# Kernel optimization log

Measured on AMD Instinct MI355X. Metric: run time of the kernel, lower is better.

## Reference

```python
import jax, jax.numpy as jnp
import numpy as np
import math

D_MODEL = 768
D_STATE = 16
EXPAND = 2
D_CONV = 4
D_INNER = EXPAND * D_MODEL  # 1536
DT_RANK = math.ceil(D_MODEL / 16)  # 48
BATCH = 2
SEQ = 2048


def setup_inputs() -> dict:
    key = jax.random.key(0)
    ks = jax.random.split(key, 9)
    s = lambda fan_in: 1.0 / np.sqrt(fan_in)
    x = jax.random.normal(ks[0], (BATCH, SEQ, D_MODEL), dtype=jnp.float32)
    W_in = jax.random.normal(ks[1], (D_MODEL, 2 * D_INNER), dtype=jnp.float32) * s(D_MODEL)
    conv_w = jax.random.normal(ks[2], (D_INNER, 1, D_CONV), dtype=jnp.float32) * s(D_CONV)
    conv_b = jax.random.normal(ks[3], (D_INNER,), dtype=jnp.float32) * s(D_CONV)
    W_x = jax.random.normal(ks[4], (D_INNER, DT_RANK + 2 * D_STATE), dtype=jnp.float32) * s(D_INNER)
    W_dt = jax.random.normal(ks[5], (DT_RANK, D_INNER), dtype=jnp.float32) * s(DT_RANK)
    b_dt = jax.random.normal(ks[6], (D_INNER,), dtype=jnp.float32) * s(DT_RANK)
    A_log = jnp.log(jnp.tile(jnp.arange(1, D_STATE + 1, dtype=jnp.float32), (D_INNER, 1)))
    Dp = jnp.ones((D_INNER,), dtype=jnp.float32)
    W_out = jax.random.normal(ks[7], (D_INNER, D_MODEL), dtype=jnp.float32) * s(D_INNER)
    return {"x": x, "W_in": W_in, "conv_w": conv_w, "conv_b": conv_b,
            "W_x": W_x, "W_dt": W_dt, "b_dt": b_dt, "A_log": A_log,
            "Dp": Dp, "W_out": W_out}


def _mamba_forward(x, W_in, conv_w, conv_b, W_x, W_dt, b_dt, A_log, Dp, W_out):
    B, L, _ = x.shape
    xz = x @ W_in                                   # [B,L,2E]
    u, res = jnp.split(xz, [D_INNER], axis=-1)      # [B,L,E] each

    # Depthwise causal conv1d (padding=d_conv-1 on the left, truncated to L)
    u_ncl = jnp.transpose(u, (0, 2, 1))             # [B,E,L]
    u_ncl = jax.lax.conv_general_dilated(
        u_ncl, conv_w,
        window_strides=(1,), padding=[(D_CONV - 1, 0)],
        dimension_numbers=("NCH", "OIH", "NCH"),
        feature_group_count=D_INNER)
    u_ncl = u_ncl + conv_b[None, :, None]
    u = jnp.transpose(u_ncl, (0, 2, 1))             # [B,L,E]
    u = jax.nn.silu(u)

    ssm = u @ W_x                                   # [B,L,R+2N]
    dt_raw, Bm, Cm = jnp.split(ssm, [DT_RANK, DT_RANK + D_STATE], axis=-1)
    dt = jax.nn.softplus(dt_raw @ W_dt + b_dt)      # [B,L,E]

    A = -jnp.exp(A_log)                             # [E,N]
    dA = jnp.exp(dt[..., None] * A)                 # [B,L,E,N]
    dBu = dt[..., None] * Bm[:, :, None, :] * u[..., None]  # [B,L,E,N]

    # Sequential SSM recurrence: h_t = dA_t * h_{t-1} + dBu_t; y_t = <h_t, C_t>
    def step(h, inp):
        dA_t, dBu_t, C_t = inp                      # [B,E,N],[B,E,N],[B,N]
        h = dA_t * h + dBu_t
        y_t = jnp.sum(h * C_t[:, None, :], axis=-1)  # [B,E]
        return h, y_t

    h0 = jnp.zeros((B, D_INNER, D_STATE), dtype=u.dtype)
    xs = (jnp.transpose(dA, (1, 0, 2, 3)),
          jnp.transpose(dBu, (1, 0, 2, 3)),
          jnp.transpose(Cm, (1, 0, 2)))
    _, ys = jax.lax.scan(step, h0, xs)              # [L,B,E]
    y = jnp.transpose(ys, (1, 0, 2))                # [B,L,E]

    y = y + u * Dp
    y = y * jax.nn.silu(res)
    return y @ W_out                                # [B,L,d_model]


def reference(x, W_in, conv_w, conv_b, W_x, W_dt, b_dt, A_log, Dp, W_out):
    return _mamba_forward(x, W_in, conv_w, conv_b, W_x, W_dt, b_dt, A_log, Dp, W_out)
```

## Files before the change

kernel.cpp:

```cpp
#include <hip/hip_runtime.h>
#include <hip/hip_bf16.h>
#include <math.h>

#define D_MODEL 768
#define D_STATE 16
#define D_CONV  4
#define D_INNER 1536
#define DT_RANK 48
#define BATCH   2
#define SEQ     2048
#define BL      (BATCH*SEQ)
#define XZ_W    (2*D_INNER)
#define SSM_W   (DT_RANK + 2*D_STATE)
#define BC_W    (2*D_STATE)
#define KSPLIT  12

#define NREC    (BATCH*D_INNER*D_STATE)
#define EG      (D_INNER/128)
#define CH      64
#define CT      32

typedef __attribute__((ext_vector_type(8))) short short8;
typedef __attribute__((ext_vector_type(4))) float f32x4;

__device__ __forceinline__ float silu_f(float x) { return x / (1.f + __expf(-x)); }
__device__ __forceinline__ float softplus_f(float x) {
    return fmaxf(x, 0.f) + log1pf(__expf(-fabsf(x)));
}

__device__ __forceinline__ void qpow8(float q, int half, float* qp)
{
    qp[0] = q;
    qp[1] = q * q;
    qp[2] = qp[1] * q;
    qp[3] = qp[1] * qp[1];
    qp[4] = qp[3] * q;
    qp[5] = qp[3] * qp[1];
    qp[6] = qp[3] * qp[2];
    qp[7] = qp[3] * qp[3];
    float s = half ? qp[7] : 1.0f;
    #pragma unroll
    for (int n = 0; n < 8; ++n) qp[n] *= s;
}

#define GLOAD16(g, l)                                                          \
    __builtin_amdgcn_global_load_lds(                                          \
        (const __attribute__((address_space(1))) unsigned int*)(g),            \
        (__attribute__((address_space(3))) unsigned int*)(l), 16, 0, 0)

#define GEMM128_BODY(A, Bt, K)                                                 \
    __shared__ __hip_bfloat16 As[128 * 32];                                    \
    __shared__ __hip_bfloat16 Bs[128 * 32];                                    \
    const int t    = threadIdx.x;                                              \
    const int wave = t >> 6;                                                   \
    const int lane = t & 63;                                                   \
    const int m0 = blockIdx.y * 128, n0 = blockIdx.x * 128;                    \
    const int wm = (wave >> 1) * 64, wn = (wave & 1) * 64;                     \
    const int l  = lane & 15, kq = lane >> 4;                                  \
    const int arow = t >> 2;                                                   \
    const int aoff = (t & 3) << 3;                                             \
    const __hip_bfloat16* gA = A  + (size_t)(m0 + arow) * K + aoff;            \
    const __hip_bfloat16* gB = Bt + (size_t)(n0 + arow) * K + aoff;            \
    char* ldsA0 = (char*)As + wave * 1024;                                     \
    char* ldsA1 = (char*)As + 4096 + wave * 1024;                              \
    char* ldsB0 = (char*)Bs + wave * 1024;                                     \
    char* ldsB1 = (char*)Bs + 4096 + wave * 1024;                              \
    const size_t rstep = (size_t)64 * K;                                       \
    f32x4 acc[4][4] = {};                                                      \
    for (int k0 = 0; k0 < K; k0 += 32) {                                       \
        __syncthreads();                                                       \
        GLOAD16(gA + k0,         ldsA0);                                       \
        GLOAD16(gA + rstep + k0, ldsA1);                                       \
        GLOAD16(gB + k0,         ldsB0);                                       \
        GLOAD16(gB + rstep + k0, ldsB1);                                       \
        __syncthreads();                                                       \
        short8 af[4], bf[4];                                                   \
        _Pragma("unroll")                                                      \
        for (int i = 0; i < 4; ++i)                                            \
            af[i] = *(const short8*)(As + (wm + i * 16 + l) * 32 + kq * 8);    \
        _Pragma("unroll")                                                      \
        for (int j = 0; j < 4; ++j)                                            \
            bf[j] = *(const short8*)(Bs + (wn + j * 16 + l) * 32 + kq * 8);    \
        _Pragma("unroll")                                                      \
        for (int i = 0; i < 4; ++i)                                            \
            _Pragma("unroll")                                                  \
            for (int j = 0; j < 4; ++j)                                        \
                acc[i][j] = __builtin_amdgcn_mfma_f32_16x16x32_bf16(           \
                    af[i], bf[j], acc[i][j], 0, 0, 0);                         \
    }

__global__ __launch_bounds__(256)
void gemm128_in(const __hip_bfloat16* __restrict__ A,
                const __hip_bfloat16* __restrict__ Bt,
                __hip_bfloat16* __restrict__ U,
                __hip_bfloat16* __restrict__ Rb, int K)
{
    GEMM128_BODY(A, Bt, K)
    #pragma unroll
    for (int i = 0; i < 4; ++i)
        #pragma unroll
        for (int j = 0; j < 4; ++j)
            #pragma unroll
            for (int r = 0; r < 4; ++r) {
                int row = m0 + wm + i * 16 + kq * 4 + r;
                int col = n0 + wn + j * 16 + l;
                float v = acc[i][j][r];
                if (col < D_INNER)
                    U[(size_t)row * D_INNER + col] = __float2bfloat16(v);
                else
                    Rb[(size_t)row * D_INNER + col - D_INNER] =
                        __float2bfloat16(silu_f(v));
            }
}

__global__ __launch_bounds__(256)
void gemm128_sp(const __hip_bfloat16* __restrict__ A,
                const __hip_bfloat16* __restrict__ Bt,
                __hip_bfloat16* __restrict__ C,
                const float* __restrict__ bias, int K)
{
    GEMM128_BODY(A, Bt, K)
    #pragma unroll
    for (int i = 0; i < 4; ++i)
        #pragma unroll
        for (int j = 0; j < 4; ++j)
            #pragma unroll
            for (int r = 0; r < 4; ++r) {
                int row = m0 + wm + i * 16 + kq * 4 + r;
                int col = n0 + wn + j * 16 + l;
                C[(size_t)row * D_INNER + col] =
                    __float2bfloat16(softplus_f(acc[i][j][r] + bias[col]));
            }
}

__global__ __launch_bounds__(256)
void gemm64_splitk(const __hip_bfloat16* __restrict__ A,
                   const __hip_bfloat16* __restrict__ Bt,
                   float* __restrict__ P, int lda, int Ksub, int ldP, int nG)
{
    __shared__ __hip_bfloat16 As[64 * 32];
    __shared__ __hip_bfloat16 Bs[128 * 32];
    const int t    = threadIdx.x;
    const int wave = t >> 6;
    const int lane = t & 63;
    const int m0 = blockIdx.y * 64, n0 = blockIdx.x * 128;
    const int wm = (wave >> 1) * 32, wn = (wave & 1) * 64;
    const int l  = lane & 15, kq = lane >> 4;
    const int kb = blockIdx.z * Ksub;

    const int arow = t >> 2;
    const int aoff = (t & 3) << 3;
    const __hip_bfloat16* gA = A  + (size_t)(m0 + arow) * lda + kb + aoff;
    const __hip_bfloat16* gB = Bt + (size_t)(n0 + arow) * lda + kb + aoff;
    char* ldsA  = (char*)As + wave * 1024;
    char* ldsB0 = (char*)Bs + wave * 1024;
    char* ldsB1 = (char*)Bs + 4096 + wave * 1024;
    const size_t rstep = (size_t)64 * lda;

    f32x4 acc[2][4] = {};

    for (int k0 = 0; k0 < Ksub; k0 += 32) {
        __syncthreads();
        GLOAD16(gA + k0,         ldsA);
        GLOAD16(gB + k0,         ldsB0);
        GLOAD16(gB + rstep + k0, ldsB1);
        __syncthreads();

        short8 af[2], bf[4];
        #pragma unroll
        for (int i = 0; i < 2; ++i)
            af[i] = *(const short8*)(As + (wm + i * 16 + l) * 32 + kq * 8);
        #pragma unroll
        for (int j = 0; j < 4; ++j)
            bf[j] = *(const short8*)(Bs + (wn + j * 16 + l) * 32 + kq * 8);
        #pragma unroll
        for (int i = 0; i < 2; ++i)
            #pragma unroll
            for (int j = 0; j < 4; ++j)
                acc[i][j] = __builtin_amdgcn_mfma_f32_16x16x32_bf16(
                    af[i], bf[j], acc[i][j], 0, 0, 0);
    }

    float* Pz = P + (size_t)blockIdx.z * BL * ldP;
    #pragma unroll
    for (int i = 0; i < 2; ++i)
        #pragma unroll
        for (int j = 0; j < 4; ++j)
            #pragma unroll
            for (int r = 0; r < 4; ++r) {
                int row = m0 + wm + i * 16 + kq * 4 + r;
                int col = n0 + wn + j * 16 + l;
                if (col < nG)
                    Pz[(size_t)row * ldP + col] = acc[i][j][r];
            }
}

__global__ __launch_bounds__(256)
void combine_ssm(const float* __restrict__ Pk,
                 __hip_bfloat16* __restrict__ dtrawb, float* __restrict__ bcb)
{
    int idx = blockIdx.x * 256 + threadIdx.x;
    int row = idx / SSM_W, col = idx % SSM_W;
    float s = 0.f;
    #pragma unroll
    for (int z = 0; z < KSPLIT; ++z)
        s += Pk[(size_t)z * BL * SSM_W + idx];
    if (col < DT_RANK) {
        dtrawb[(size_t)row * 64 + col] = __float2bfloat16(s);
    } else {
        bcb[(size_t)row * BC_W + col - DT_RANK] = s;
        if (col < 64) dtrawb[(size_t)row * 64 + col] = __float2bfloat16(0.f);
    }
}

__global__ __launch_bounds__(256)
void prep_all(const float* __restrict__ x, const float* __restrict__ W_in,
              const float* __restrict__ W_x, const float* __restrict__ W_dt,
              const float* __restrict__ W_out,
              __hip_bfloat16* __restrict__ xb, __hip_bfloat16* __restrict__ wint,
              __hip_bfloat16* __restrict__ WxT, __hip_bfloat16* __restrict__ WdtT,
              __hip_bfloat16* __restrict__ wott)
{
    __shared__ float tile[32][33];
    int bid = blockIdx.x;
    const int tid = threadIdx.x;

    if (bid < 3072) {
        int i = bid * 256 + tid;
        float4 v = ((const float4*)x)[i];
        union { ushort4 u; __hip_bfloat16 h[4]; } p;
        p.h[0] = __float2bfloat16(v.x);
        p.h[1] = __float2bfloat16(v.y);
        p.h[2] = __float2bfloat16(v.z);
        p.h[3] = __float2bfloat16(v.w);
        ((ushort4*)xb)[i] = p.u;
        return;
    }
    bid -= 3072;
    if (bid < 384) {
        int idx = bid * 256 + tid;
        int n = idx >> 6, k = idx & 63;
        float v = (k < DT_RANK) ? W_dt[(size_t)k * D_INNER + n] : 0.f;
        WdtT[idx] = __float2bfloat16(v);
        return;
    }
    bid -= 384;
    const float* W; __hip_bfloat16* Wt; int R, C_in, lda, gx;
    if (bid < 2304)      { W = W_in;  Wt = wint; R = D_MODEL; C_in = XZ_W;    lda = XZ_W;    gx = 96; }
    else if (bid < 2448) { bid -= 2304; W = W_x;  Wt = WxT;  R = D_INNER; C_in = SSM_W;   lda = SSM_W;   gx = 3;  }
    else                 { bid -= 2448; W = W_out; Wt = wott; R = D_INNER; C_in = D_MODEL; lda = D_MODEL; gx = 24; }
    int c0 = (bid % gx) * 32, r0 = (bid / gx) * 32;
    int tx = tid & 31, ty = tid >> 5;
    #pragma unroll
    for (int i = 0; i < 32; i += 8)
        tile[ty + i][tx] = (c0 + tx < C_in)
            ? W[(size_t)(r0 + ty + i) * lda + c0 + tx] : 0.f;
    __syncthreads();
    #pragma unroll
    for (int i = 0; i < 32; i += 8)
        Wt[(size_t)(c0 + ty + i) * R + r0 + tx] = __float2bfloat16(tile[tx][ty + i]);
}

__global__ __launch_bounds__(256)
void gemm_f32(const float* __restrict__ A, const float* __restrict__ B,
              float* __restrict__ C, const float* __restrict__ bias,
              int N, int K, int lda, int ldb, int ldc, int epilogue)
{
    __shared__ float As[16][64];
    __shared__ float Bs[16][64];
    const int tid = threadIdx.x;
    const int m0 = blockIdx.y * 64;
    const int n0 = blockIdx.x * 64;
    const int tx = tid & 15, ty = tid >> 4;
    const int a_row = tid >> 2;
    const int a_k4  = (tid & 3) << 2;
    const int b_k   = tid >> 4;
    const int b_n4  = (tid & 15) << 2;
    const bool full_n = (n0 + 64) <= N;

    float acc[4][4] = {};

    for (int k0 = 0; k0 < K; k0 += 16) {
        float4 av = *(const float4*)(A + (size_t)(m0 + a_row) * lda + (k0 + a_k4));
        As[a_k4 + 0][a_row] = av.x;
        As[a_k4 + 1][a_row] = av.y;
        As[a_k4 + 2][a_row] = av.z;
        As[a_k4 + 3][a_row] = av.w;
        if (full_n) {
            *(float4*)&Bs[b_k][b_n4] =
                *(const float4*)(B + (size_t)(k0 + b_k) * ldb + (n0 + b_n4));
        } else {
            #pragma unroll
            for (int j = 0; j < 4; ++j) {
                int col = n0 + b_n4 + j;
                Bs[b_k][b_n4 + j] = (col < N) ? B[(size_t)(k0 + b_k) * ldb + col] : 0.f;
            }
        }
        __syncthreads();
        #pragma unroll
        for (int kk = 0; kk < 16; ++kk) {
            float a[4], bb[4];
            #pragma unroll
            for (int i = 0; i < 4; ++i) a[i]  = As[kk][ty * 4 + i];
            #pragma unroll
            for (int j = 0; j < 4; ++j) bb[j] = Bs[kk][tx * 4 + j];
            #pragma unroll
            for (int i = 0; i < 4; ++i)
                #pragma unroll
                for (int j = 0; j < 4; ++j)
                    acc[i][j] = fmaf(a[i], bb[j], acc[i][j]);
        }
        __syncthreads();
    }

    #pragma unroll
    for (int i = 0; i < 4; ++i) {
        size_t row = (size_t)(m0 + ty * 4 + i);
        #pragma unroll
        for (int j = 0; j < 4; ++j) {
            int col = n0 + tx * 4 + j;
            if (full_n || col < N) {
                float v = acc[i][j];
                if (epilogue == 1) v = softplus_f(v + bias[col]);
                C[row * ldc + col] = v;
            }
        }
    }
}

__global__ __launch_bounds__(256)
void conv_silu(const float* __restrict__ in, const float* __restrict__ cw,
               const float* __restrict__ cb, float* __restrict__ uc32,
               __hip_bfloat16* __restrict__ ucb, int in_ld)
{
    int idx = blockIdx.x * 256 + threadIdx.x;
    int e  = idx % D_INNER;
    int bt = idx / D_INNER;
    int t  = bt % SEQ;
    const float* base = in + (size_t)bt * in_ld + e;
    float w0 = cw[e * 4 + 0], w1 = cw[e * 4 + 1], w2 = cw[e * 4 + 2], w3 = cw[e * 4 + 3];
    float acc = cb[e] + w3 * base[0];
    if (t >= 1) acc = fmaf(w2, base[-in_ld], acc);
    if (t >= 2) acc = fmaf(w1, base[-2 * in_ld], acc);
    if (t >= 3) acc = fmaf(w0, base[-3 * in_ld], acc);
    float v = silu_f(acc);
    if (uc32) uc32[(size_t)bt * D_INNER + e] = v;
    if (ucb)  ucb[(size_t)bt * D_INNER + e] = __float2bfloat16(v);
}

__global__ __launch_bounds__(256)
void conv_silu_b2(const __hip_bfloat16* __restrict__ in,
                  const float* __restrict__ cw, const float* __restrict__ cb,
                  __hip_bfloat16* __restrict__ ucb)
{
    int idx = blockIdx.x * 256 + threadIdx.x;
    int ep = idx % (D_INNER / 2);
    int bt = idx / (D_INNER / 2);
    int t  = bt % SEQ;
    int e  = ep * 2;
    const ushort2* base = (const ushort2*)(in + (size_t)bt * D_INNER + e);
    const int ld2 = D_INNER / 2;
    float4 wa = ((const float4*)cw)[e];
    float4 wb = ((const float4*)cw)[e + 1];
    float2 bias = ((const float2*)cb)[ep];

    ushort2 v0 = base[0];
    float a0 = bias.x + wa.w * __bfloat162float(*(__hip_bfloat16*)&v0.x);
    float a1 = bias.y + wb.w * __bfloat162float(*(__hip_bfloat16*)&v0.y);
    if (t >= 1) {
        ushort2 v = base[-ld2];
        a0 = fmaf(wa.z, __bfloat162float(*(__hip_bfloat16*)&v.x), a0);
        a1 = fmaf(wb.z, __bfloat162float(*(__hip_bfloat16*)&v.y), a1);
    }
    if (t >= 2) {
        ushort2 v = base[-2 * ld2];
        a0 = fmaf(wa.y, __bfloat162float(*(__hip_bfloat16*)&v.x), a0);
        a1 = fmaf(wb.y, __bfloat162float(*(__hip_bfloat16*)&v.y), a1);
    }
    if (t >= 3) {
        ushort2 v = base[-3 * ld2];
        a0 = fmaf(wa.x, __bfloat162float(*(__hip_bfloat16*)&v.x), a0);
        a1 = fmaf(wb.x, __bfloat162float(*(__hip_bfloat16*)&v.y), a1);
    }
    union { ushort2 u; __hip_bfloat16 h[2]; } p;
    p.h[0] = __float2bfloat16(silu_f(a0));
    p.h[1] = __float2bfloat16(silu_f(a1));
    ((ushort2*)ucb)[(size_t)bt * ld2 + ep] = p.u;
}

__device__ __forceinline__ float load_u(const void* uc, int u_bf16, size_t idx)
{
    return u_bf16 ? __bfloat162float(((const __hip_bfloat16*)uc)[idx])
                  : ((const float*)uc)[idx];
}

__global__ __launch_bounds__(256)
void scan_pass1(const void* __restrict__ dt, int dt_bf16, int dt_ld,
                const void* __restrict__ uc, int u_bf16,
                const float* __restrict__ bc, int bc_ld,
                float* __restrict__ Pbuf, float* __restrict__ Hend,
                int ch, int ct)
{
    __shared__ float Bs[64][16];
    const int tid  = threadIdx.x;
    const int half = tid & 1;
    const int eg   = blockIdx.x % EG;
    const int c    = (blockIdx.x / EG) % ch;
    const int b    = blockIdx.x / (EG * ch);
    const int e    = eg * 128 + (tid >> 1);
    const size_t base = (size_t)b * SEQ + (size_t)c * ct;

    for (int idx = tid; idx < ct * 16; idx += 256) {
        int tr = idx >> 4, col = idx & 15;
        Bs[tr][col] = bc[(base + tr) * bc_ld + col];
    }
    __syncthreads();

    float h[8] = {};
    float sdt = 0.f;

    #pragma unroll 4
    for (int t = 0; t < ct; ++t) {
        size_t r = base + t;
        float dt_v = load_u(dt, dt_bf16, r * dt_ld + e);
        float u_v  = load_u(uc, u_bf16, r * D_INNER + e);
        sdt += dt_v;
        float du = dt_v * u_v;
        float bl[8];
        *(float4*)&bl[0] = *(const float4*)&Bs[t][half * 8];
        *(float4*)&bl[4] = *(const float4*)&Bs[t][half * 8 + 4];
        float qp[8];
        qpow8(__expf(-dt_v), half, qp);
        #pragma unroll
        for (int n = 0; n < 8; ++n)
            h[n] = fmaf(qp[n], h[n], du * bl[n]);
    }

    float P[8];
    qpow8(__expf(-sdt), half, P);

    size_t i = (size_t)c * NREC + (size_t)(b * D_INNER + e) * D_STATE + half * 8;
    *(float4*)&Pbuf[i]     = *(float4*)&P[0];
    *(float4*)&Pbuf[i + 4] = *(float4*)&P[4];
    *(float4*)&Hend[i]     = *(float4*)&h[0];
    *(float4*)&Hend[i + 4] = *(float4*)&h[4];
}

__global__ __launch_bounds__(256)
void scan_pass2(float* __restrict__ Pbuf, float* __restrict__ Hend, int ch)
{
    size_t i = (size_t)blockIdx.x * 256 + threadIdx.x;
    float H = 0.f;
    for (int c = 0; c < ch; ++c) {
        size_t o = (size_t)c * NREC + i;
        float P  = Pbuf[o];
        float he = Hend[o];
        Pbuf[o] = H;
        H = fmaf(P, H, he);
    }
}

__global__ __launch_bounds__(256)
void scan2b(float* __restrict__ Pbuf, float* __restrict__ Hend)
{
    size_t i = (size_t)blockIdx.x * 256 + threadIdx.x;
    float H = 0.f;
    #pragma unroll
    for (int c = 0; c < CH; ++c) {
        size_t o = (size_t)c * NREC + i;
        float P  = Pbuf[o];
        float he = Hend[o];
        Pbuf[o] = H;
        H = fmaf(P, H, he);
    }
}

__global__ __launch_bounds__(256)
void scan_pass3(const void* dt, int dt_bf16, int dt_ld,
                const void* __restrict__ uc, int u_bf16,
                const float* __restrict__ bc, int bc_ld,
                const void* __restrict__ res, int res_ld, int res_presilu,
                const float* __restrict__ Hstart, void* yout, int bf16_out,
                int ch, int ct)
{
    __shared__ float BCs[64][32];
    const int tid  = threadIdx.x;
    const int half = tid & 1;
    const int eg   = blockIdx.x % EG;
    const int c    = (blockIdx.x / EG) % ch;
    const int b    = blockIdx.x / (EG * ch);
    const int e    = eg * 128 + (tid >> 1);
    const size_t base = (size_t)b * SEQ + (size_t)c * ct;

    for (int idx = tid; idx < ct * 32; idx += 256) {
        int tr = idx >> 5, col = idx & 31;
        BCs[tr][col] = bc[(base + tr) * bc_ld + col];
    }
    __syncthreads();

    float h[8];
    {
        const float* hp = Hstart + (size_t)c * NREC
                        + (size_t)(b * D_INNER + e) * D_STATE + half * 8;
        *(float4*)&h[0] = *(const float4*)hp;
        *(float4*)&h[4] = *(const float4*)(hp + 4);
    }

    #pragma unroll 4
    for (int t = 0; t < ct; ++t) {
        size_t r = base + t;
        float dt_v = load_u(dt, dt_bf16, r * dt_ld + e);
        float u_v  = load_u(uc, u_bf16, r * D_INNER + e);
        float bl[8], cl[8];
        *(float4*)&bl[0] = *(const float4*)&BCs[t][half * 8];
        *(float4*)&bl[4] = *(const float4*)&BCs[t][half * 8 + 4];
        *(float4*)&cl[0] = *(const float4*)&BCs[t][16 + half * 8];
        *(float4*)&cl[4] = *(const float4*)&BCs[t][16 + half * 8 + 4];
        float du = dt_v * u_v;
        float qp[8];
        qpow8(__expf(-dt_v), half, qp);
        float p = 0.f;
        #pragma unroll
        for (int n = 0; n < 8; ++n) {
            h[n] = fmaf(qp[n], h[n], du * bl[n]);
            p = fmaf(h[n], cl[n], p);
        }
        p += __shfl_xor(p, 1);
        if (half == 0) {
            float rs = res_presilu
                ? __bfloat162float(((const __hip_bfloat16*)res)[r * res_ld + e])
                : silu_f(((const float*)res)[r * res_ld + e]);
            float y = (p + u_v) * rs;
            if (bf16_out) ((__hip_bfloat16*)yout)[r * D_INNER + e] = __float2bfloat16(y);
            else          ((float*)yout)[r * D_INNER + e] = y;
        }
    }
}

__global__ __launch_bounds__(256)
void scan1b(const __hip_bfloat16* __restrict__ dt,
            const __hip_bfloat16* __restrict__ uc,
            const float* __restrict__ bc,
            float* __restrict__ Pbuf, float* __restrict__ Hend)
{
    __shared__ float Bs[CT][16];
    __shared__ __hip_bfloat16 DT[CT][128];
    __shared__ __hip_bfloat16 UC[CT][128];
    const int tid  = threadIdx.x;
    const int wave = tid >> 6;
    const int half = tid & 1;
    const int eg   = blockIdx.x % EG;
    const int c    = (blockIdx.x / EG) % CH;
    const int b    = blockIdx.x / (EG * CH);
    const int el   = tid >> 1;
    const int e    = eg * 128 + el;
    const size_t base = (size_t)b * SEQ + (size_t)c * CT;

    {
        const int rs = tid >> 4;
        const int c8 = (tid & 15) << 3;
        const __hip_bfloat16* gdt = dt + (base + rs) * D_INNER + eg * 128 + c8;
        const __hip_bfloat16* guc = uc + (base + rs) * D_INNER + eg * 128 + c8;
        char* ldt = (char*)DT + wave * 1024;
        char* luc = (char*)UC + wave * 1024;
        GLOAD16(gdt,                 ldt);
        GLOAD16(gdt + 16 * D_INNER,  ldt + 4096);
        GLOAD16(guc,                 luc);
        GLOAD16(guc + 16 * D_INNER,  luc + 4096);
    }
    for (int idx = tid; idx < CT * 16; idx += 256) {
        int tr = idx >> 4, col = idx & 15;
        Bs[tr][col] = bc[(base + tr) * BC_W + col];
    }
    __syncthreads();

    float h[8] = {};
    float sdt = 0.f;

    #pragma unroll 4
    for (int t = 0; t < CT; ++t) {
        float dt_v = __bfloat162float(DT[t][el]);
        float u_v  = __bfloat162float(UC[t][el]);
        sdt += dt_v;
        float du = dt_v * u_v;
        float bl[8];
        *(float4*)&bl[0] = *(const float4*)&Bs[t][half * 8];
        *(float4*)&bl[4] = *(const float4*)&Bs[t][half * 8 + 4];
        float qp[8];
        qpow8(__expf(-dt_v), half, qp);
        #pragma unroll
        for (int n = 0; n < 8; ++n)
            h[n] = fmaf(qp[n], h[n], du * bl[n]);
    }

    float P[8];
    qpow8(__expf(-sdt), half, P);

    size_t i = (size_t)c * NREC + (size_t)(b * D_INNER + e) * D_STATE + half * 8;
    *(float4*)&Pbuf[i]     = *(float4*)&P[0];
    *(float4*)&Pbuf[i + 4] = *(float4*)&P[4];
    *(float4*)&Hend[i]     = *(float4*)&h[0];
    *(float4*)&Hend[i + 4] = *(float4*)&h[4];
}

__global__ __launch_bounds__(256)
void scan3b(const __hip_bfloat16* __restrict__ dt,
            const __hip_bfloat16* __restrict__ uc,
            const float* __restrict__ bc,
            const __hip_bfloat16* __restrict__ res,
            const float* __restrict__ Hstart,
            __hip_bfloat16* __restrict__ yout)
{
    __shared__ float BCs[CT][32];
    __shared__ __hip_bfloat16 DT[CT][128];
    __shared__ __hip_bfloat16 UC[CT][128];
    __shared__ __hip_bfloat16 RS[CT][128];
    const int tid  = threadIdx.x;
    const int wave = tid >> 6;
    const int half = tid & 1;
    const int eg   = blockIdx.x % EG;
    const int c    = (blockIdx.x / EG) % CH;
    const int b    = blockIdx.x / (EG * CH);
    const int el   = tid >> 1;
    const int e    = eg * 128 + el;
    const size_t base = (size_t)b * SEQ + (size_t)c * CT;

    {
        const int rs = tid >> 4;
        const int c8 = (tid & 15) << 3;
        const __hip_bfloat16* gdt = dt  + (base + rs) * D_INNER + eg * 128 + c8;
        const __hip_bfloat16* guc = uc  + (base + rs) * D_INNER + eg * 128 + c8;
        const __hip_bfloat16* grs = res + (base + rs) * D_INNER + eg * 128 + c8;
        char* ldt = (char*)DT + wave * 1024;
        char* luc = (char*)UC + wave * 1024;
        char* lrs = (char*)RS + wave * 1024;
        GLOAD16(gdt,                ldt);
        GLOAD16(gdt + 16 * D_INNER, ldt + 4096);
        GLOAD16(guc,                luc);
        GLOAD16(guc + 16 * D_INNER, luc + 4096);
        GLOAD16(grs,                lrs);
        GLOAD16(grs + 16 * D_INNER, lrs + 4096);
    }
    for (int idx = tid; idx < CT * 32; idx += 256) {
        int tr = idx >> 5, col = idx & 31;
        BCs[tr][col] = bc[(base + tr) * BC_W + col];
    }

    float h[8];
    {
        const float* hp = Hstart + (size_t)c * NREC
                        + (size_t)(b * D_INNER + e) * D_STATE + half * 8;
        *(float4*)&h[0] = *(const float4*)hp;
        *(float4*)&h[4] = *(const float4*)(hp + 4);
    }
    __syncthreads();

    #pragma unroll 4
    for (int t = 0; t < CT; ++t) {
        size_t r = base + t;
        float dt_v = __bfloat162float(DT[t][el]);
        float u_v  = __bfloat162float(UC[t][el]);
        float bl[8], cl[8];
        *(float4*)&bl[0] = *(const float4*)&BCs[t][half * 8];
        *(float4*)&bl[4] = *(const float4*)&BCs[t][half * 8 + 4];
        *(float4*)&cl[0] = *(const float4*)&BCs[t][16 + half * 8];
        *(float4*)&cl[4] = *(const float4*)&BCs[t][16 + half * 8 + 4];
        float du = dt_v * u_v;
        float qp[8];
        qpow8(__expf(-dt_v), half, qp);
        float p = 0.f;
        #pragma unroll
        for (int n = 0; n < 8; ++n) {
            h[n] = fmaf(qp[n], h[n], du * bl[n]);
            p = fmaf(h[n], cl[n], p);
        }
        p += __shfl_xor(p, 1);
        if (half == 0) {
            float rs = __bfloat162float(RS[t][el]);
            float y  = (p + u_v) * rs;
            yout[r * D_INNER + e] = __float2bfloat16(y);
        }
    }
}

extern "C" void kernel_launch(void* const* d_in, const int* in_sizes, int n_in,
                              void* d_out, int out_size, void* d_ws, size_t ws_size,
                              hipStream_t stream)
{
    const float* x      = (const float*)d_in[0];
    const float* W_in   = (const float*)d_in[1];
    const float* conv_w = (const float*)d_in[2];
    const float* conv_b = (const float*)d_in[3];
    const float* W_x    = (const float*)d_in[4];
    const float* W_dt   = (const float*)d_in[5];
    const float* b_dt   = (const float*)d_in[6];
    const float* W_out  = (const float*)d_in[9];
    float* out = (float*)d_out;
    char*  ws  = (char*)d_ws;

    const bool fast = ws_size >= (size_t)104660992;

    if (fast) {
        __hip_bfloat16* ub   = (__hip_bfloat16*)(ws);
        __hip_bfloat16* yb   = (__hip_bfloat16*)(ws);
        __hip_bfloat16* srb  = (__hip_bfloat16*)(ws + 25165824);
        __hip_bfloat16* ucb  = (__hip_bfloat16*)(ws + 37748736);
        __hip_bfloat16* dtbb = (__hip_bfloat16*)(ws + 50331648);
        __hip_bfloat16* xb   = (__hip_bfloat16*)(ws + 50331648);
        __hip_bfloat16* wint = (__hip_bfloat16*)(ws + 56623104);
        float* Pk   = (float*)(ws + 75497472);
        float* Pbuf = (float*)(ws + 75497472);
        float* Hend = (float*)(ws + 88080384);
        __hip_bfloat16* WxT  = (__hip_bfloat16*)(ws + 100663296);
        __hip_bfloat16* dtrawb = (__hip_bfloat16*)(ws + 101056512);
        __hip_bfloat16* WdtT = (__hip_bfloat16*)(ws + 101580800);
        float* bcb  = (float*)(ws + 101777408);
        __hip_bfloat16* wott = (__hip_bfloat16*)(ws + 102301696);

        const int scan_grid = BATCH * CH * EG;

        prep_all<<<7056, 256, 0, stream>>>(
            x, W_in, W_x, W_dt, W_out, xb, wint, WxT, WdtT, wott);

        gemm128_in<<<dim3(XZ_W / 128, BL / 128), 256, 0, stream>>>(
            xb, wint, ub, srb, D_MODEL);

        conv_silu_b2<<<(BL * D_INNER / 2) / 256, 256, 0, stream>>>(
            ub, conv_w, conv_b, ucb);

        gemm64_splitk<<<dim3(1, BL / 64, KSPLIT), 256, 0, stream>>>(
            ucb, WxT, Pk, D_INNER, 128, SSM_W, SSM_W);
        combine_ssm<<<(BL * SSM_W) / 256, 256, 0, stream>>>(Pk, dtrawb, bcb);

        gemm128_sp<<<dim3(D_INNER / 128, BL / 128), 256, 0, stream>>>(
            dtrawb, WdtT, dtbb, b_dt, 64);

        scan1b<<<scan_grid, 256, 0, stream>>>(dtbb, ucb, bcb, Pbuf, Hend);
        scan2b<<<NREC / 256, 256, 0, stream>>>(Pbuf, Hend);
        scan3b<<<scan_grid, 256, 0, stream>>>(dtbb, ucb, bcb, srb, Pbuf, yb);

        gemm64_splitk<<<dim3(D_MODEL / 128, BL / 64, 1), 256, 0, stream>>>(
            yb, wott, out, D_INNER, D_INNER, D_MODEL, D_MODEL);
    } else {
        float* xz  = (float*)(ws);
        float* uc  = (float*)(ws + 50331648);
        float* smb = (float*)(ws + 75497472);
        float* dtb = (float*)(ws + 76808192);
        float* yf  = dtb;
        float* Pbuf = out;
        float* Hend = out + (size_t)32 * NREC;
        const int scan_grid = BATCH * 32 * EG;
        gemm_f32<<<dim3(XZ_W / 64, BL / 64), 256, 0, stream>>>(
            x, W_in, xz, nullptr, XZ_W, D_MODEL, D_MODEL, XZ_W, XZ_W, 0);
        conv_silu<<<(BL * D_INNER) / 256, 256, 0, stream>>>(
            xz, conv_w, conv_b, uc, nullptr, XZ_W);
        gemm_f32<<<dim3(2, BL / 64), 256, 0, stream>>>(
            uc, W_x, smb, nullptr, SSM_W, D_INNER, D_INNER, SSM_W, SSM_W, 0);
        gemm_f32<<<dim3(D_INNER / 64, BL / 64), 256, 0, stream>>>(
            smb, W_dt, dtb, b_dt, D_INNER, DT_RANK, SSM_W, D_INNER, D_INNER, 1);
        scan_pass1<<<scan_grid, 256, 0, stream>>>(
            (const void*)dtb, 0, D_INNER, (const void*)uc, 0, smb + DT_RANK, SSM_W,
            Pbuf, Hend, 32, SEQ / 32);
        scan_pass2<<<NREC / 256, 256, 0, stream>>>(Pbuf, Hend, 32);
        scan_pass3<<<scan_grid, 256, 0, stream>>>(
            (const void*)dtb, 0, D_INNER, (const void*)uc, 0, smb + DT_RANK, SSM_W,
            (const void*)(xz + D_INNER), XZ_W, 0, Pbuf, (void*)yf, 0, 32, SEQ / 32);
        gemm_f32<<<dim3(D_MODEL / 64, BL / 64), 256, 0, stream>>>(
            yf, W_out, out, nullptr, D_MODEL, D_INNER, D_INNER, D_MODEL, D_MODEL, 0);
    }
}
```

Measured before the change: 272.5 us.

## Fold chunk-carry scan into pass-3 with early exit; add XCD block swizzle

Removes the separate scan2b kernel that propagated chunk-boundary states. Each pass-3 thread now rebuilds its starting state by walking backwards over earlier chunks' Hend/Pbuf, and stops once the accumulated decay product underflows below a small threshold. This saves a kernel launch and a full read/write pass over Pbuf, but adds redundant backward reads that grow with chunk index, and relies on the decay becoming negligible, which is approximate. Separately, the GEMM kernels remap block indices so neighbouring tiles are grouped onto the same XCD for better L2 reuse.

```diff
diff --git a/kernel.cpp b/kernel.cpp
--- a/kernel.cpp
+++ b/kernel.cpp
@@ -48,13 +48,21 @@
         (const __attribute__((address_space(1))) unsigned int*)(g),            \
         (__attribute__((address_space(3))) unsigned int*)(l), 16, 0, 0)
 
+#define XCD_SWZ_XY()                                                           \
+    const int nwg_ = gridDim.x * gridDim.y;                                    \
+    const int id_  = blockIdx.y * gridDim.x + blockIdx.x;                      \
+    const int sw_  = (id_ & 7) * (nwg_ >> 3) + (id_ >> 3);                     \
+    const int bx_  = sw_ % gridDim.x;                                          \
+    const int by_  = sw_ / gridDim.x;
+
 #define GEMM128_BODY(A, Bt, K)                                                 \
     __shared__ __hip_bfloat16 As[128 * 32];                                    \
     __shared__ __hip_bfloat16 Bs[128 * 32];                                    \
     const int t    = threadIdx.x;                                              \
     const int wave = t >> 6;                                                   \
     const int lane = t & 63;                                                   \
-    const int m0 = blockIdx.y * 128, n0 = blockIdx.x * 128;                    \
+    XCD_SWZ_XY()                                                               \
+    const int m0 = by_ * 128, n0 = bx_ * 128;                                  \
     const int wm = (wave >> 1) * 64, wn = (wave & 1) * 64;                     \
     const int l  = lane & 15, kq = lane >> 4;                                  \
     const int arow = t >> 2;                                                   \
@@ -143,7 +151,8 @@
     const int t    = threadIdx.x;
     const int wave = t >> 6;
     const int lane = t & 63;
-    const int m0 = blockIdx.y * 64, n0 = blockIdx.x * 128;
+    XCD_SWZ_XY()
+    const int m0 = by_ * 64, n0 = bx_ * 128;
     const int wm = (wave >> 1) * 32, wn = (wave & 1) * 64;
     const int l  = lane & 15, kq = lane >> 4;
     const int kb = blockIdx.z * Ksub;
@@ -461,21 +470,6 @@
 }
 
 __global__ __launch_bounds__(256)
-void scan2b(float* __restrict__ Pbuf, float* __restrict__ Hend)
-{
-    size_t i = (size_t)blockIdx.x * 256 + threadIdx.x;
-    float H = 0.f;
-    #pragma unroll
-    for (int c = 0; c < CH; ++c) {
-        size_t o = (size_t)c * NREC + i;
-        float P  = Pbuf[o];
-        float he = Hend[o];
-        Pbuf[o] = H;
-        H = fmaf(P, H, he);
-    }
-}
-
-__global__ __launch_bounds__(256)
 void scan_pass3(const void* dt, int dt_bf16, int dt_ld,
                 const void* __restrict__ uc, int u_bf16,
                 const float* __restrict__ bc, int bc_ld,
@@ -604,11 +598,12 @@
 }
 
 __global__ __launch_bounds__(256)
-void scan3b(const __hip_bfloat16* __restrict__ dt,
+void scan3c(const __hip_bfloat16* __restrict__ dt,
             const __hip_bfloat16* __restrict__ uc,
             const float* __restrict__ bc,
             const __hip_bfloat16* __restrict__ res,
-            const float* __restrict__ Hstart,
+            const float* __restrict__ Pbuf,
+            const float* __restrict__ Hend,
             __hip_bfloat16* __restrict__ yout)
 {
     __shared__ float BCs[CT][32];
@@ -646,12 +641,24 @@
         BCs[tr][col] = bc[(base + tr) * BC_W + col];
     }
 
-    float h[8];
+    float h[8] = {};
     {
-        const float* hp = Hstart + (size_t)c * NREC
-                        + (size_t)(b * D_INNER + e) * D_STATE + half * 8;
-        *(float4*)&h[0] = *(const float4*)hp;
-        *(float4*)&h[4] = *(const float4*)(hp + 4);
+        const size_t sidx = (size_t)(b * D_INNER + e) * D_STATE + half * 8;
+        float f[8] = {1.f, 1.f, 1.f, 1.f, 1.f, 1.f, 1.f, 1.f};
+        for (int cp = c - 1; cp >= 0; --cp) {
+            size_t o = (size_t)cp * NREC + sidx;
+            float he[8], pp[8];
+            *(float4*)&he[0] = *(const float4*)(Hend + o);
+            *(float4*)&he[4] = *(const float4*)(Hend + o + 4);
+            *(float4*)&pp[0] = *(const float4*)(Pbuf + o);
+            *(float4*)&pp[4] = *(const float4*)(Pbuf + o + 4);
+            #pragma unroll
+            for (int n = 0; n < 8; ++n) {
+                h[n] = fmaf(f[n], he[n], h[n]);
+                f[n] *= pp[n];
+            }
+            if (!__any(f[0] > 1e-35f)) break;
+        }
     }
     __syncthreads();
 
@@ -736,8 +743,7 @@
             dtrawb, WdtT, dtbb, b_dt, 64);
 
         scan1b<<<scan_grid, 256, 0, stream>>>(dtbb, ucb, bcb, Pbuf, Hend);
-        scan2b<<<NREC / 256, 256, 0, stream>>>(Pbuf, Hend);
-        scan3b<<<scan_grid, 256, 0, stream>>>(dtbb, ucb, bcb, srb, Pbuf, yb);
+        scan3c<<<scan_grid, 256, 0, stream>>>(dtbb, ucb, bcb, srb, Pbuf, Hend, yb);
 
         gemm64_splitk<<<dim3(D_MODEL / 128, BL / 64, 1), 256, 0, stream>>>(
             yb, wott, out, D_INNER, D_INNER, D_MODEL, D_MODEL);
```

After: 266.0 us. -2.4%, faster.
